# Optimization experiments

Hardware: AMD Instinct MI355X
Metric: run time of the kernel (lower is better)

The kernel has to match this reference:

```python
import jax, jax.numpy as jnp
import numpy as np


def pfaffian(A):
    """Pfaffian of even-dim skew-symmetric A via Parlett-Reid LTL^T (no pivoting).
    pf(A) = prod over elimination steps of the (k, k+1) pivot."""
    n = A.shape[0]
    ar = jnp.arange(n)

    def step(carry, i):
        A, pf = carry
        k = 2 * i
        pivot = A[k, k + 1]
        mask = ar > (k + 1)                      # rows/cols k+2:
        tau = jnp.where(mask, A[k, :], 0.0) / pivot
        col = jnp.where(mask, A[:, k + 1], 0.0)
        # rank-2 skew update of the trailing submatrix
        A = A + tau[:, None] * col[None, :] - col[:, None] * tau[None, :]
        return (A, pf * pivot), None

    (A, pf), _ = jax.lax.scan(step, (A, jnp.ones((), A.dtype)), jnp.arange(n // 2))
    return pf


def setup_inputs() -> dict:
    key = jax.random.key(0)
    k1, k2 = jax.random.split(key)
    N = 128          # nsites; Nparticle = N (spin system, one particle per site)
    B = 128          # batch of Monte-Carlo configurations
    x = jax.random.normal(k1, (B, N), jnp.float32)
    scale = np.float32(np.sqrt(np.e / N))
    F = jax.random.normal(k2, (N * (2 * N - 1),), jnp.float32) * scale
    return {"x": x, "F": F}


def reference(x, F):
    N = x.shape[-1]
    Nparticle = N
    twoN = 2 * N
    # scatter parameter vector into strict lower triangle, antisymmetrize
    F_full = jnp.zeros((twoN, twoN), F.dtype).at[jnp.tril_indices(twoN, -1)].set(F)
    F_full = F_full - F_full.T

    def single(xi):
        # spin system: up orbitals where x>0, down orbitals where x<=0
        occ = jnp.concatenate([xi > 0, xi <= 0])
        idx = jnp.flatnonzero(occ, size=Nparticle)
        A = F_full[idx[:, None], idx[None, :]]   # [Nparticle, Nparticle] gather
        return pfaffian(A)

    return jax.vmap(single)(x)
```

## Files before the change

kernel.cpp:

```cpp
#include <hip/hip_runtime.h>


#define POFF(i) ((i) + (((i) >> 5) << 2))
#define RL(v, l) __int_as_float(__builtin_amdgcn_readlane(__float_as_int(v), (l)))

__global__ __launch_bounds__(512) void pfaffian_kernel(
    const float* __restrict__ x,
    const float* __restrict__ F,
    float* __restrict__ out)
{
    const int b    = blockIdx.x;
    const int t    = threadIdx.x;
    const int lane = t & 63;
    const int wave = t >> 6;

    __shared__ int idx_sh[128];
    __shared__ int wtot[4];
    __shared__ __align__(16) float tauLDS[2][4][144];
    __shared__ __align__(16) float colLDS[2][4][144];
    __shared__ __align__(16) float rS[2][4][144];
    __shared__ __align__(16) float cS[2][4][144];

    if (t < 256) {
        const float xv  = x[b * 128 + (t & 127)];
        const bool  pos = xv > 0.0f;
        const bool  o   = (t < 128) ? pos : !pos;
        const unsigned long long mm = __ballot(o);
        const int rank = __popcll(mm & ((1ull << lane) - 1ull));
        if (lane == 63) wtot[wave] = rank + (o ? 1 : 0);
        __syncthreads();
        int off = 0;
#pragma unroll
        for (int w = 0; w < 4; ++w)
            if (w < wave) off += wtot[w];
        if (o) idx_sh[off + rank] = t;
    } else {
        __syncthreads();
    }
    __syncthreads();

    const int m = (wave == 0) ? 0 : (wave <= 3 ? 8 - wave : wave - 3);

    const int rg   = (m << 2) | ((t >> 4) & 3);
    const int cg   = t & 15;
    const int row0 = rg << 2;
    const int col0 = cg << 3;
    const int prow = POFF(row0);
    const int pcol = POFF(col0);

    auto Fval = [&](int gi, int gj) -> float {
        const int ii = idx_sh[gi];
        const int jj = idx_sh[gj];
        if (ii == jj) return 0.0f;
        const int hi = ii > jj ? ii : jj;
        const int lo = ii > jj ? jj : ii;
        const float v = F[(hi * (hi - 1)) / 2 + lo];
        return (ii < jj) ? -v : v;
    };

    float A[4][8];
    if (wave >= 1) {
        int ri[4], ci[8];
#pragma unroll
        for (int a = 0; a < 4; ++a) ri[a] = idx_sh[row0 + a];
#pragma unroll
        for (int c = 0; c < 8; ++c) ci[c] = idx_sh[col0 + c];
#pragma unroll
        for (int a = 0; a < 4; ++a) {
            const int ii = ri[a];
#pragma unroll
            for (int c = 0; c < 8; ++c) {
                const int jj = ci[c];
                const int hi = ii > jj ? ii : jj;
                const int lo = ii > jj ? jj : ii;
                float v = (ii == jj) ? 0.0f : F[(hi * (hi - 1)) / 2 + lo];
                A[a][c] = (ii < jj) ? -v : v;
            }
        }
    }

    auto stage = [&](int Pn, int st) {
        const int rgbase = 2 * Pn;
        if (rg == rgbase) {
            *(float4*)&rS[st][0][pcol]     = make_float4(A[0][0], A[0][1], A[0][2], A[0][3]);
            *(float4*)&rS[st][0][pcol + 4] = make_float4(A[0][4], A[0][5], A[0][6], A[0][7]);
            *(float4*)&rS[st][1][pcol]     = make_float4(A[2][0], A[2][1], A[2][2], A[2][3]);
            *(float4*)&rS[st][1][pcol + 4] = make_float4(A[2][4], A[2][5], A[2][6], A[2][7]);
        }
        if (rg == rgbase + 1) {
            *(float4*)&rS[st][2][pcol]     = make_float4(A[0][0], A[0][1], A[0][2], A[0][3]);
            *(float4*)&rS[st][2][pcol + 4] = make_float4(A[0][4], A[0][5], A[0][6], A[0][7]);
            *(float4*)&rS[st][3][pcol]     = make_float4(A[2][0], A[2][1], A[2][2], A[2][3]);
            *(float4*)&rS[st][3][pcol + 4] = make_float4(A[2][4], A[2][5], A[2][6], A[2][7]);
        }
        if (cg == Pn) {
            *(float4*)&cS[st][0][prow] = make_float4(A[0][1], A[1][1], A[2][1], A[3][1]);
            *(float4*)&cS[st][1][prow] = make_float4(A[0][3], A[1][3], A[2][3], A[3][3]);
            *(float4*)&cS[st][2][prow] = make_float4(A[0][5], A[1][5], A[2][5], A[3][5]);
            *(float4*)&cS[st][3][prow] = make_float4(A[0][7], A[1][7], A[2][7], A[3][7]);
        }
    };

    float pf = 1.0f;

    auto crew2 = [&](int Pn, bool pre) {
        const int sv = Pn & 1;
        const int g0 = lane << 1;
        const int g1 = g0 + 1;
        const int pg = POFF(g0);
        float R[4][2], C[4][2];
#pragma unroll
        for (int j = 0; j < 4; ++j) {
            const float2 rv = *(const float2*)&rS[sv][j][pg];
            const float2 cv = *(const float2*)&cS[sv][j][pg];
            R[j][0] = rv.x; R[j][1] = rv.y;
            C[j][0] = cv.x; C[j][1] = cv.y;
        }
        if (pre) {
            const int svp  = sv ^ 1;
            const int base = POFF(8 * Pn);
            float4 Tq[4][2], Cq[4][2];
#pragma unroll
            for (int jp = 0; jp < 4; ++jp) {
                Tq[jp][0] = *(const float4*)&tauLDS[svp][jp][base];
                Tq[jp][1] = *(const float4*)&tauLDS[svp][jp][base + 4];
                Cq[jp][0] = *(const float4*)&colLDS[svp][jp][base];
                Cq[jp][1] = *(const float4*)&colLDS[svp][jp][base + 4];
            }
#pragma unroll
            for (int jp = 0; jp < 4; ++jp) {
                const float trA[4] = {Tq[jp][0].x, Tq[jp][0].z, Tq[jp][1].x, Tq[jp][1].z};
                const float crA[4] = {Cq[jp][0].x, Cq[jp][0].z, Cq[jp][1].x, Cq[jp][1].z};
                const float tcA[4] = {Tq[jp][0].y, Tq[jp][0].w, Tq[jp][1].y, Tq[jp][1].w};
                const float ccA[4] = {Cq[jp][0].y, Cq[jp][0].w, Cq[jp][1].y, Cq[jp][1].w};
                const float2 tpv = *(const float2*)&tauLDS[svp][jp][pg];
                const float2 cpv = *(const float2*)&colLDS[svp][jp][pg];
#pragma unroll
                for (int a = 0; a < 4; ++a) {
                    const float tau_r = trA[a];
                    const float col_r = crA[a];
                    R[a][0] = __fmaf_rn(-col_r, tpv.x,
                              __fmaf_rn(tau_r, cpv.x, R[a][0]));
                    R[a][1] = __fmaf_rn(-col_r, tpv.y,
                              __fmaf_rn(tau_r, cpv.y, R[a][1]));
                    const float tau_c = tcA[a];
                    const float col_c = ccA[a];
                    C[a][0] = __fmaf_rn(-cpv.x, tau_c,
                              __fmaf_rn(tpv.x, col_c, C[a][0]));
                    C[a][1] = __fmaf_rn(-cpv.y, tau_c,
                              __fmaf_rn(tpv.y, col_c, C[a][1]));
                }
            }
        }
        float TAU[4][2], CV[4][2];
#pragma unroll
        for (int j = 0; j < 4; ++j) {
            const int k = 8 * Pn + 2 * j;
            const float piv = RL(R[j][1], 4 * Pn + j);
            pf = __fmul_rn(pf, piv);
            TAU[j][0] = (g0 > k + 1) ? __fdiv_rn(R[j][0], piv) : 0.0f;
            TAU[j][1] = (g1 > k + 1) ? __fdiv_rn(R[j][1], piv) : 0.0f;
            CV[j][0]  = (g0 > k + 1) ? C[j][0] : 0.0f;
            CV[j][1]  = (g1 > k + 1) ? C[j][1] : 0.0f;
            *(float2*)&tauLDS[sv][j][pg] = make_float2(TAU[j][0], TAU[j][1]);
            *(float2*)&colLDS[sv][j][pg] = make_float2(CV[j][0], CV[j][1]);
#pragma unroll
            for (int j2 = j + 1; j2 < 4; ++j2) {
                const int ls = 4 * Pn + j2;
                const float tau_r = RL(TAU[j][0], ls);
                const float col_r = RL(CV[j][0], ls);
                R[j2][0] = __fmaf_rn(-col_r, TAU[j][0],
                           __fmaf_rn(tau_r, CV[j][0], R[j2][0]));
                R[j2][1] = __fmaf_rn(-col_r, TAU[j][1],
                           __fmaf_rn(tau_r, CV[j][1], R[j2][1]));
                const float tau_c = RL(TAU[j][1], ls);
                const float col_c = RL(CV[j][1], ls);
                C[j2][0] = __fmaf_rn(-CV[j][0], tau_c,
                           __fmaf_rn(TAU[j][0], col_c, C[j2][0]));
                C[j2][1] = __fmaf_rn(-CV[j][1], tau_c,
                           __fmaf_rn(TAU[j][1], col_c, C[j2][1]));
            }
        }
    };

    if (wave == 0) {
        const int c0 = lane << 1;
        const int pc = POFF(c0);
#pragma unroll
        for (int st = 0; st < 2; ++st) {
#pragma unroll
            for (int j = 0; j < 4; ++j) {
                const int k = 8 * st + 2 * j;
                float2 rv, cv;
                rv.x = Fval(k, c0);
                rv.y = Fval(k, c0 + 1);
                cv.x = Fval(c0, k + 1);
                cv.y = Fval(c0 + 1, k + 1);
                *(float2*)&rS[st][j][pc] = rv;
                *(float2*)&cS[st][j][pc] = cv;
            }
        }
        crew2(0, false);
    }
    __syncthreads();

    for (int P = 0; P < 15; ++P) {
        if (wave >= 1 && P < 2 * m) {
            const int sp = P & 1;
#pragma unroll
            for (int j = 0; j < 4; ++j) {
                const float4 trv = *(const float4*)&tauLDS[sp][j][prow];
                const float4 crv = *(const float4*)&colLDS[sp][j][prow];
                const float4 t0v = *(const float4*)&tauLDS[sp][j][pcol];
                const float4 t1v = *(const float4*)&tauLDS[sp][j][pcol + 4];
                const float4 c0v = *(const float4*)&colLDS[sp][j][pcol];
                const float4 c1v = *(const float4*)&colLDS[sp][j][pcol + 4];
                const float tr[4] = {trv.x, trv.y, trv.z, trv.w};
                const float cr[4] = {crv.x, crv.y, crv.z, crv.w};
                const float tc[8] = {t0v.x, t0v.y, t0v.z, t0v.w,
                                     t1v.x, t1v.y, t1v.z, t1v.w};
                const float cc[8] = {c0v.x, c0v.y, c0v.z, c0v.w,
                                     c1v.x, c1v.y, c1v.z, c1v.w};
#pragma unroll
                for (int a = 0; a < 4; ++a) {
#pragma unroll
                    for (int c = 0; c < 8; ++c) {
                        A[a][c] = __fmaf_rn(-cr[a], tc[c],
                                  __fmaf_rn(tr[a], cc[c], A[a][c]));
                    }
                }
            }
            if (P <= 13) stage(P + 2, P & 1);
        }
        if (wave == 0) crew2(P + 1, true);
        __syncthreads();
    }

    if (t == 0) out[b] = pf;
}

extern "C" void kernel_launch(void* const* d_in, const int* in_sizes, int n_in,
                              void* d_out, int out_size, void* d_ws, size_t ws_size,
                              hipStream_t stream) {
    const float* x = (const float*)d_in[0];
    const float* F = (const float*)d_in[1];
    float* out     = (float*)d_out;
    (void)in_sizes; (void)n_in; (void)out_size; (void)d_ws; (void)ws_size;

    pfaffian_kernel<<<128, 512, 0, stream>>>(x, F, out);
}
```

Measured before the change: 77.10 us.

## Split trailing-matrix update across 16 waves with one panel per wave

The block grows from 512 to 1024 threads. Each thread now owns a 2x8 tile instead of 4x8, so each wave maps to one 8-row panel, and waves drop out of the rank-2 update loop as their panel is eliminated. The old paired triangular load-balancing scheme is removed. Register pressure and per-thread FMA work are halved, and more waves are available per CU to hide latency, since only 128 blocks run. The cost is more waves taking part in every barrier. Separately, the pivot division is replaced by one reciprocal followed by multiplies.

Result: no change. 78.38 us (+1.7%).

```diff
diff --git a/kernel.cpp b/kernel.cpp
--- a/kernel.cpp
+++ b/kernel.cpp
@@ -4,7 +4,7 @@
 #define POFF(i) ((i) + (((i) >> 5) << 2))
 #define RL(v, l) __int_as_float(__builtin_amdgcn_readlane(__float_as_int(v), (l)))
 
-__global__ __launch_bounds__(512) void pfaffian_kernel(
+__global__ __launch_bounds__(1024) void pfaffian_kernel(
     const float* __restrict__ x,
     const float* __restrict__ F,
     float* __restrict__ out)
@@ -39,14 +39,11 @@
     }
     __syncthreads();
 
-    const int m = (wave == 0) ? 0 : (wave <= 3 ? 8 - wave : wave - 3);
-
-    const int rg   = (m << 2) | ((t >> 4) & 3);
-    const int cg   = t & 15;
-    const int row0 = rg << 2;
-    const int col0 = cg << 3;
-    const int prow = POFF(row0);
-    const int pcol = POFF(col0);
+    const int rg    = t >> 4;
+    const int cg    = t & 15;
+    const int col0  = cg << 3;
+    const int prow2 = POFF(rg << 1);
+    const int pcol  = POFF(col0);
 
     auto Fval = [&](int gi, int gj) -> float {
         const int ii = idx_sh[gi];
@@ -58,15 +55,15 @@
         return (ii < jj) ? -v : v;
     };
 
-    float A[4][8];
-    if (wave >= 1) {
-        int ri[4], ci[8];
-#pragma unroll
-        for (int a = 0; a < 4; ++a) ri[a] = idx_sh[row0 + a];
+    float A[2][8];
+    if (wave >= 2) {
+        int ri[2], ci[8];
+#pragma unroll
+        for (int a = 0; a < 2; ++a) ri[a] = idx_sh[(rg << 1) + a];
 #pragma unroll
         for (int c = 0; c < 8; ++c) ci[c] = idx_sh[col0 + c];
 #pragma unroll
-        for (int a = 0; a < 4; ++a) {
+        for (int a = 0; a < 2; ++a) {
             const int ii = ri[a];
 #pragma unroll
             for (int c = 0; c < 8; ++c) {
@@ -80,24 +77,16 @@
     }
 
     auto stage = [&](int Pn, int st) {
-        const int rgbase = 2 * Pn;
-        if (rg == rgbase) {
-            *(float4*)&rS[st][0][pcol]     = make_float4(A[0][0], A[0][1], A[0][2], A[0][3]);
-            *(float4*)&rS[st][0][pcol + 4] = make_float4(A[0][4], A[0][5], A[0][6], A[0][7]);
-            *(float4*)&rS[st][1][pcol]     = make_float4(A[2][0], A[2][1], A[2][2], A[2][3]);
-            *(float4*)&rS[st][1][pcol + 4] = make_float4(A[2][4], A[2][5], A[2][6], A[2][7]);
-        }
-        if (rg == rgbase + 1) {
-            *(float4*)&rS[st][2][pcol]     = make_float4(A[0][0], A[0][1], A[0][2], A[0][3]);
-            *(float4*)&rS[st][2][pcol + 4] = make_float4(A[0][4], A[0][5], A[0][6], A[0][7]);
-            *(float4*)&rS[st][3][pcol]     = make_float4(A[2][0], A[2][1], A[2][2], A[2][3]);
-            *(float4*)&rS[st][3][pcol + 4] = make_float4(A[2][4], A[2][5], A[2][6], A[2][7]);
+        const int q = rg - 4 * Pn;
+        if (q >= 0 && q < 4) {
+            *(float4*)&rS[st][q][pcol]     = make_float4(A[0][0], A[0][1], A[0][2], A[0][3]);
+            *(float4*)&rS[st][q][pcol + 4] = make_float4(A[0][4], A[0][5], A[0][6], A[0][7]);
         }
         if (cg == Pn) {
-            *(float4*)&cS[st][0][prow] = make_float4(A[0][1], A[1][1], A[2][1], A[3][1]);
-            *(float4*)&cS[st][1][prow] = make_float4(A[0][3], A[1][3], A[2][3], A[3][3]);
-            *(float4*)&cS[st][2][prow] = make_float4(A[0][5], A[1][5], A[2][5], A[3][5]);
-            *(float4*)&cS[st][3][prow] = make_float4(A[0][7], A[1][7], A[2][7], A[3][7]);
+            *(float2*)&cS[st][0][prow2] = make_float2(A[0][1], A[1][1]);
+            *(float2*)&cS[st][1][prow2] = make_float2(A[0][3], A[1][3]);
+            *(float2*)&cS[st][2][prow2] = make_float2(A[0][5], A[1][5]);
+            *(float2*)&cS[st][3][prow2] = make_float2(A[0][7], A[1][7]);
         }
     };
 
@@ -158,8 +147,9 @@
             const int k = 8 * Pn + 2 * j;
             const float piv = RL(R[j][1], 4 * Pn + j);
             pf = __fmul_rn(pf, piv);
-            TAU[j][0] = (g0 > k + 1) ? __fdiv_rn(R[j][0], piv) : 0.0f;
-            TAU[j][1] = (g1 > k + 1) ? __fdiv_rn(R[j][1], piv) : 0.0f;
+            const float rp = __fdiv_rn(1.0f, piv);
+            TAU[j][0] = (g0 > k + 1) ? __fmul_rn(R[j][0], rp) : 0.0f;
+            TAU[j][1] = (g1 > k + 1) ? __fmul_rn(R[j][1], rp) : 0.0f;
             CV[j][0]  = (g0 > k + 1) ? C[j][0] : 0.0f;
             CV[j][1]  = (g1 > k + 1) ? C[j][1] : 0.0f;
             *(float2*)&tauLDS[sv][j][pg] = make_float2(TAU[j][0], TAU[j][1]);
@@ -205,24 +195,24 @@
     __syncthreads();
 
     for (int P = 0; P < 15; ++P) {
-        if (wave >= 1 && P < 2 * m) {
+        if (wave >= P + 2) {
             const int sp = P & 1;
 #pragma unroll
             for (int j = 0; j < 4; ++j) {
-                const float4 trv = *(const float4*)&tauLDS[sp][j][prow];
-                const float4 crv = *(const float4*)&colLDS[sp][j][prow];
+                const float2 trv = *(const float2*)&tauLDS[sp][j][prow2];
+                const float2 crv = *(const float2*)&colLDS[sp][j][prow2];
                 const float4 t0v = *(const float4*)&tauLDS[sp][j][pcol];
                 const float4 t1v = *(const float4*)&tauLDS[sp][j][pcol + 4];
                 const float4 c0v = *(const float4*)&colLDS[sp][j][pcol];
                 const float4 c1v = *(const float4*)&colLDS[sp][j][pcol + 4];
-                const float tr[4] = {trv.x, trv.y, trv.z, trv.w};
-                const float cr[4] = {crv.x, crv.y, crv.z, crv.w};
+                const float tr[2] = {trv.x, trv.y};
+                const float cr[2] = {crv.x, crv.y};
                 const float tc[8] = {t0v.x, t0v.y, t0v.z, t0v.w,
                                      t1v.x, t1v.y, t1v.z, t1v.w};
                 const float cc[8] = {c0v.x, c0v.y, c0v.z, c0v.w,
                                      c1v.x, c1v.y, c1v.z, c1v.w};
 #pragma unroll
-                for (int a = 0; a < 4; ++a) {
+                for (int a = 0; a < 2; ++a) {
 #pragma unroll
                     for (int c = 0; c < 8; ++c) {
                         A[a][c] = __fmaf_rn(-cr[a], tc[c],
@@ -247,5 +237,5 @@
     float* out     = (float*)d_out;
     (void)in_sizes; (void)n_in; (void)out_size; (void)d_ws; (void)ws_size;
 
-    pfaffian_kernel<<<128, 512, 0, stream>>>(x, F, out);
+    pfaffian_kernel<<<128, 1024, 0, stream>>>(x, F, out);
 }
```
